# Kernel tuning notes

Hardware: AMD Instinct MI355X
Metric: run time of the kernel (lower is better)

Reference implementation:

```python
import jax, jax.numpy as jnp
import numpy as np

B, T, HS, H, R = 4, 2048, 1024, 16, 16
D = HS // H  # 64 head_dim
LOGIT_01 = float(np.log(0.1 / 0.9))    # g_proj bias init
LOGIT_098 = float(np.log(0.98 / 0.02)) # base decay logits init


def _rope_cos_sin(seq_len, dim, base=10000.0):
    half = dim // 2
    inv_freq = 1.0 / (base ** (jnp.arange(half, dtype=jnp.float32) / half))
    freqs = jnp.arange(seq_len, dtype=jnp.float32)[:, None] * inv_freq[None, :]  # [T, half]
    return jnp.cos(freqs), jnp.sin(freqs)


def _apply_rope(x, cos, sin):
    # x: [B,T,H,D] with D even; rotate interleaved pairs over full D
    c = cos[None, :, None, :]
    s = sin[None, :, None, :]
    x1 = x[..., 0::2]
    x2 = x[..., 1::2]
    r1 = x1 * c - x2 * s
    r2 = x1 * s + x2 * c
    return jnp.stack((r1, r2), axis=-1).reshape(x.shape)


def setup_inputs() -> dict:
    key = jax.random.key(0)
    ks = jax.random.split(key, 10)
    def rn(k, shape, s=0.02):
        return jax.random.normal(k, shape, dtype=jnp.float32) * s
    return {
        "x": jax.random.normal(ks[0], (B, T, HS), dtype=jnp.float32),
        "q_w": rn(ks[1], (HS, HS)),
        "k_w": rn(ks[2], (HS, HS)),
        "v_w": rn(ks[3], (HS, HS)),
        "Wq": rn(ks[4], (H, R, D), 0.05),
        "Wk": rn(ks[5], (H, R, D), 0.05),
        "g_w": rn(ks[6], (H * R, HS)),
        "g_b": jnp.full((H * R,), LOGIT_01, dtype=jnp.float32),
        "base_decay_logits": jnp.full((H, R), LOGIT_098, dtype=jnp.float32),
        "out_w": rn(ks[7], (HS, HS)),
        "out_b": jnp.zeros((HS,), dtype=jnp.float32),
        "ln_g": jnp.ones((HS,), dtype=jnp.float32),
        "ln_b": jnp.zeros((HS,), dtype=jnp.float32),
    }


def reference(x, q_w, k_w, v_w, Wq, Wk, g_w, g_b, base_decay_logits,
              out_w, out_b, ln_g, ln_b):
    b, t, hs = x.shape
    h, r, d = Wq.shape
    # qkv projections (torch Linear: x @ W.T)
    q = (x @ q_w.T).reshape(b, t, h, d)
    k = (x @ k_w.T).reshape(b, t, h, d)
    v = (x @ v_w.T).reshape(b, t, h, d)
    # RoPE (dim_rot == head_dim since it is even)
    cos, sin = _rope_cos_sin(t, d)
    q = _apply_rope(q, cos, sin)
    k = _apply_rope(k, cos, sin)
    # low-rank projections
    q_r = jnp.einsum('bthd,hrd->bthr', q, Wq)
    k_r = jnp.einsum('bthd,hrd->bthr', k, Wk)
    # content gates
    g = jax.nn.sigmoid((x @ g_w.T + g_b).reshape(b, t, h, r))
    decay = jax.nn.sigmoid(base_decay_logits)[None, :, :, None]  # [1,H,r,1]
    scale = 1.0 / jnp.sqrt(jnp.asarray(d, dtype=x.dtype))

    def step(M, inp):
        q_t, k_t, v_t, g_t = inp  # [B,H,r], [B,H,r], [B,H,D], [B,H,r]
        M = M * decay + jnp.einsum('bhr,bhd->bhrd', g_t * k_t * scale, v_t)
        y = jnp.einsum('bhr,bhrd->bhd', q_t, M)
        return M, y

    xs = (q_r.transpose(1, 0, 2, 3), k_r.transpose(1, 0, 2, 3),
          v.transpose(1, 0, 2, 3), g.transpose(1, 0, 2, 3))
    M0 = jnp.zeros((b, h, r, d), dtype=x.dtype)
    _, Y = jax.lax.scan(step, M0, xs)  # Y: [T,B,H,D]
    Y = Y.transpose(1, 0, 2, 3).reshape(b, t, hs)
    out = Y @ out_w.T + out_b  # dropout is identity at eval time
    hres = x + out
    mu = jnp.mean(hres, axis=-1, keepdims=True)
    var = jnp.mean((hres - mu) ** 2, axis=-1, keepdims=True)
    return (hres - mu) / jnp.sqrt(var + 1e-5) * ln_g + ln_b
```

## Files before the change

kernel.cpp:

```cpp
#include <hip/hip_runtime.h>
#include <hip/hip_bf16.h>

#define B_ 4
#define T_ 2048
#define HS_ 1024
#define H_ 16
#define R_ 16
#define D_ 64
#define BT_ (B_*T_)
#define NC_ 3328
#define CHUNK_ 64
#define NCHUNK_ (T_/CHUNK_)

typedef __attribute__((ext_vector_type(8))) short short8;
typedef __attribute__((ext_vector_type(4))) float f32x4;

__device__ __forceinline__ float b2f(ushort u){
    union{unsigned int i; float f;} v; v.i = ((unsigned int)u) << 16; return v.f;
}
__device__ __forceinline__ ushort f2b(float f){
    __hip_bfloat16 h = __float2bfloat16(f);
    return *reinterpret_cast<ushort*>(&h);
}
__device__ __forceinline__ float sigm(float x){ return 1.f/(1.f+expf(-x)); }

__device__ __forceinline__ void gl_lds16(const void* g, void* l){
    __builtin_amdgcn_global_load_lds((const __attribute__((address_space(1))) void*)g,
                                     (__attribute__((address_space(3))) void*)l,
                                     16, 0, 0);
}

__global__ void k_cast4(const float* __restrict__ src, ushort* __restrict__ dst){
    int i = blockIdx.x*256 + threadIdx.x;
    float4 v = ((const float4*)src)[i];
    ushort4 o; o.x=f2b(v.x); o.y=f2b(v.y); o.z=f2b(v.z); o.w=f2b(v.w);
    ((ushort4*)dst)[i] = o;
}

__global__ void k_build_wcat(const float* __restrict__ qw, const float* __restrict__ kw,
                             const float* __restrict__ vw, const float* __restrict__ gw,
                             ushort* __restrict__ wcat){
    int i = blockIdx.x*256 + threadIdx.x;
    int e = i*4;
    int row = e >> 10, col = e & 1023;
    const float* src;
    if      (row < 1024) src = qw + (size_t)row*1024 + col;
    else if (row < 2048) src = kw + (size_t)(row-1024)*1024 + col;
    else if (row < 3072) src = vw + (size_t)(row-2048)*1024 + col;
    else                 src = gw + (size_t)(row-3072)*1024 + col;
    float4 v = *(const float4*)src;
    ushort4 o; o.x=f2b(v.x); o.y=f2b(v.y); o.z=f2b(v.z); o.w=f2b(v.w);
    ((ushort4*)wcat)[i] = o;
}

__global__ void k_rope_tab(float* __restrict__ cosT, float* __restrict__ sinT){
    int i = blockIdx.x*256 + threadIdx.x;
    int t = i >> 5, f = i & 31;
    float inv = powf(10000.f, -(float)f/32.f);
    float a = (float)t * inv;
    cosT[i] = cosf(a);
    sinT[i] = sinf(a);
}

__global__ __launch_bounds__(512, 2) void k_gemm256(const ushort* __restrict__ A,
                                                    const ushort* __restrict__ Bm,
                                                    ushort* __restrict__ C,
                                                    int K, int ldc){
    __shared__ __align__(16) ushort lds[65536];
    const int tid  = threadIdx.x;
    const int lane = tid & 63, w = tid >> 6;
    const int fr = lane & 15, fg = lane >> 4;
    const int wm = w >> 2, wn = w & 3;
    const int qa = (fg + (fr >> 1)) & 3;

    int mt = gridDim.x;
    int L = blockIdx.y * mt + blockIdx.x;
    int bxi, byi;
    int msub = mt >> 3;
    if((mt & 7) == 0 && msub > 0){
        int xcd = L & 7, c = L >> 3;
        bxi = xcd * msub + (c % msub);
        byi = c / msub;
    } else { bxi = blockIdx.x; byi = blockIdx.y; }
    const long arow0 = (long)bxi * 256;
    const long brow0 = (long)byi * 256;

    const int srow = tid >> 2;
    const int scol = ((((tid & 3) - (tid >> 3)) & 3)) * 8;
    const ushort* gsrc[4];
    gsrc[0] = A  + (arow0 +       srow) * (size_t)K + scol;
    gsrc[1] = A  + (arow0 + 128 + srow) * (size_t)K + scol;
    gsrc[2] = Bm + (brow0 +       srow) * (size_t)K + scol;
    gsrc[3] = Bm + (brow0 + 128 + srow) * (size_t)K + scol;

#define STG(s, l) gl_lds16(gsrc[l] + (size_t)(s)*32, \
                           &lds[((s)&3)*16384 + (l)*4096 + w*512])

    f32x4 acc[8][4];
#pragma unroll
    for(int m=0;m<8;m++)
#pragma unroll
        for(int n=0;n<4;n++)
            acc[m][n] = (f32x4){0.f,0.f,0.f,0.f};

    const int NT = K >> 6;
#pragma unroll
    for(int s=0; s<3; ++s)
#pragma unroll
        for(int l=0; l<4; ++l) STG(s, l);

    short8 bv[4];
    for(int t=0; t<NT; ++t){
#pragma unroll
        for(int ph=0; ph<4; ++ph){
            const int ks = ph >> 1, mh = ph & 1;
            if(mh == 0) asm volatile("s_waitcnt vmcnt(8)" ::: "memory");
            __builtin_amdgcn_s_barrier();
            __builtin_amdgcn_sched_barrier(0);
            {
                const int s = 2*t + 3 + ks;
                const int l0 = mh*2;
                STG(s, l0);
                STG(s, l0+1);
            }
            const int sb = ((2*t + ks) & 3) * 16384;
            if(mh == 0){
#pragma unroll
                for(int nf=0; nf<4; ++nf){
                    int rb = (wn&1)*64 + nf*16 + fr;
                    bv[nf] = *(const short8*)&lds[sb + 8192 + rb*32 + qa*8];
                }
            }
            short8 af[4];
#pragma unroll
            for(int mm=0; mm<4; ++mm){
                int ra = wm*128 + (mh*4+mm)*16 + fr;
                af[mm] = *(const short8*)&lds[sb + ra*32 + qa*8];
            }
            __builtin_amdgcn_s_setprio(1);
#pragma unroll
            for(int mm=0; mm<4; ++mm)
#pragma unroll
            for(int nf=0; nf<4; ++nf)
                acc[mh*4+mm][nf] = __builtin_amdgcn_mfma_f32_16x16x32_bf16(
                    af[mm], bv[nf], acc[mh*4+mm][nf], 0,0,0);
            __builtin_amdgcn_s_setprio(0);
        }
    }
#undef STG
    asm volatile("s_waitcnt vmcnt(0)" ::: "memory");

#pragma unroll
    for(int m=0;m<8;m++)
#pragma unroll
        for(int n=0;n<4;n++){
            long col = brow0 + wn*64 + n*16 + fr;
#pragma unroll
            for(int j=0;j<4;j++){
                long row = arow0 + wm*128 + m*16 + fg*4 + j;
                C[row*(size_t)ldc + col] = f2b(acc[m][n][j]);
            }
        }
}

__global__ __launch_bounds__(256) void k_gemm_bt(const ushort* __restrict__ A,
                                                 const ushort* __restrict__ Bm,
                                                 ushort* __restrict__ C,
                                                 int K, int ldc){
    __shared__ __align__(16) ushort Asl[128*32];
    __shared__ __align__(16) ushort Bsl[128*32];
    int tid  = threadIdx.x;
    int lane = tid & 63, wid = tid >> 6;
    int wrow = (wid >> 1)*64, wcol = (wid & 1)*64;
    long arow0 = (long)blockIdx.x * 128;
    long brow0 = (long)blockIdx.y * 128;

    int srow = tid >> 2, sseg = (tid & 3)*8;
    const ushort* ga0 = A  + (arow0      + srow)*(size_t)K + sseg;
    const ushort* ga1 = ga0 + 64*(size_t)K;
    const ushort* gb0 = Bm + (brow0      + srow)*(size_t)K + sseg;
    const ushort* gb1 = gb0 + 64*(size_t)K;
    ushort* la0 = &Asl[(tid>>6)*512];
    ushort* la1 = la0 + 2048;
    ushort* lb0 = &Bsl[(tid>>6)*512];
    ushort* lb1 = lb0 + 2048;

    f32x4 acc[4][4];
#pragma unroll
    for(int m=0;m<4;m++)
#pragma unroll
        for(int n=0;n<4;n++)
            acc[m][n] = (f32x4){0.f,0.f,0.f,0.f};

    int fr = lane & 15, fg = lane >> 4;
    for(int kt=0; kt<K; kt+=32){
        __syncthreads();
        gl_lds16(ga0 + kt, la0);
        gl_lds16(ga1 + kt, la1);
        gl_lds16(gb0 + kt, lb0);
        gl_lds16(gb1 + kt, lb1);
        __syncthreads();

        short8 af[4], bfr[4];
#pragma unroll
        for(int m=0;m<4;m++) af[m]  = *(const short8*)&Asl[(wrow + m*16 + fr)*32 + fg*8];
#pragma unroll
        for(int n=0;n<4;n++) bfr[n] = *(const short8*)&Bsl[(wcol + n*16 + fr)*32 + fg*8];
#pragma unroll
        for(int m=0;m<4;m++)
#pragma unroll
            for(int n=0;n<4;n++)
                acc[m][n] = __builtin_amdgcn_mfma_f32_16x16x32_bf16(af[m], bfr[n], acc[m][n], 0,0,0);
    }

#pragma unroll
    for(int m=0;m<4;m++)
#pragma unroll
        for(int n=0;n<4;n++){
            long col = brow0 + wcol + n*16 + fr;
#pragma unroll
            for(int j=0;j<4;j++){
                long row = arow0 + wrow + m*16 + fg*4 + j;
                C[row*(long)ldc + col] = f2b(acc[m][n][j]);
            }
        }
}

__global__ __launch_bounds__(256) void k_rope_proj(const ushort* __restrict__ qkvg,
                                                   const float* __restrict__ cosT,
                                                   const float* __restrict__ sinT,
                                                   const float* __restrict__ Wq,
                                                   const float* __restrict__ Wk,
                                                   const float* __restrict__ gb,
                                                   float* __restrict__ qr_s,
                                                   float* __restrict__ gk_s){
    __shared__ __align__(16) ushort lq[64*72], lk[64*72];
    __shared__ __align__(16) ushort wql[16*72], wkl[16*72];
    int tid = threadIdx.x, wid = tid >> 6, lane = tid & 63;
    int bt0 = blockIdx.x * 64;
    int h   = blockIdx.y;

    {
        int row = tid >> 4, seg = tid & 15;
        float4 wq4 = *(const float4*)(Wq + (size_t)h*1024 + row*64 + seg*4);
        float4 wk4 = *(const float4*)(Wk + (size_t)h*1024 + row*64 + seg*4);
        ushort* dq = &wql[row*72 + seg*4];
        ushort* dk = &wkl[row*72 + seg*4];
        dq[0]=f2b(wq4.x); dq[1]=f2b(wq4.y); dq[2]=f2b(wq4.z); dq[3]=f2b(wq4.w);
        dk[0]=f2b(wk4.x); dk[1]=f2b(wk4.y); dk[2]=f2b(wk4.z); dk[3]=f2b(wk4.w);
    }

#pragma unroll
    for(int rep=0; rep<2; ++rep){
        int flat = rep*256 + tid;
        int row = flat >> 3, seg = flat & 7;
        int t = (bt0 + row) & 2047;
        const ushort* base = qkvg + (size_t)(bt0+row)*NC_ + h*64 + seg*8;
        short8 q8 = *(const short8*)base;
        short8 k8 = *(const short8*)(base + 1024);
        float4 cv = *(const float4*)&cosT[t*32 + seg*4];
        float4 sv = *(const float4*)&sinT[t*32 + seg*4];
        float qf[8], kf[8];
#pragma unroll
        for(int j=0;j<8;j++){ qf[j]=b2f((ushort)q8[j]); kf[j]=b2f((ushort)k8[j]); }
        float c4[4] = {cv.x,cv.y,cv.z,cv.w};
        float s4[4] = {sv.x,sv.y,sv.z,sv.w};
        short8 qo, ko;
#pragma unroll
        for(int p=0;p<4;p++){
            float c=c4[p], s=s4[p];
            qo[2*p]   = (short)f2b(qf[2*p]*c - qf[2*p+1]*s);
            qo[2*p+1] = (short)f2b(qf[2*p]*s + qf[2*p+1]*c);
            ko[2*p]   = (short)f2b(kf[2*p]*c - kf[2*p+1]*s);
            ko[2*p+1] = (short)f2b(kf[2*p]*s + kf[2*p+1]*c);
        }
        *(short8*)&lq[row*72 + seg*8] = qo;
        *(short8*)&lk[row*72 + seg*8] = ko;
    }
    __syncthreads();

    int fr = lane & 15, fg = lane >> 4;
    int wrow = wid*16;
    short8 aq0 = *(const short8*)&lq[(wrow+fr)*72 + fg*8];
    short8 aq1 = *(const short8*)&lq[(wrow+fr)*72 + 32 + fg*8];
    short8 ak0 = *(const short8*)&lk[(wrow+fr)*72 + fg*8];
    short8 ak1 = *(const short8*)&lk[(wrow+fr)*72 + 32 + fg*8];
    short8 bq0 = *(const short8*)&wql[fr*72 + fg*8];
    short8 bq1 = *(const short8*)&wql[fr*72 + 32 + fg*8];
    short8 bk0 = *(const short8*)&wkl[fr*72 + fg*8];
    short8 bk1 = *(const short8*)&wkl[fr*72 + 32 + fg*8];
    f32x4 accq = (f32x4){0.f,0.f,0.f,0.f};
    f32x4 acck = (f32x4){0.f,0.f,0.f,0.f};
    accq = __builtin_amdgcn_mfma_f32_16x16x32_bf16(aq0, bq0, accq, 0,0,0);
    accq = __builtin_amdgcn_mfma_f32_16x16x32_bf16(aq1, bq1, accq, 0,0,0);
    acck = __builtin_amdgcn_mfma_f32_16x16x32_bf16(ak0, bk0, acck, 0,0,0);
    acck = __builtin_amdgcn_mfma_f32_16x16x32_bf16(ak1, bk1, acck, 0,0,0);

    int r = fr;
    float gbv = gb[h*16 + r];
#pragma unroll
    for(int j=0;j<4;j++){
        int bt = bt0 + wrow + fg*4 + j;
        int t  = bt & 2047, b = bt >> 11;
        size_t o = (((size_t)(b*16 + h))*2048 + t)*16 + r;
        qr_s[o] = accq[j];
        float gl = b2f(qkvg[(size_t)bt*NC_ + 3072 + h*16 + r]) + gbv;
        gk_s[o] = sigm(gl) * acck[j] * 0.125f;
    }
}

__global__ __launch_bounds__(64) void k_scan_local(const ushort* __restrict__ qkvg,
                                                   const float* __restrict__ gk_s,
                                                   const float* __restrict__ bdl,
                                                   float* __restrict__ Mloc){
    int lane = threadIdx.x;
    int bx = blockIdx.x;
    int ch = bx & (NCHUNK_-1), bh = bx >> 5;
    int b = bh >> 4, h = bh & 15;
    float dec[16], M[16];
#pragma unroll
    for(int r=0;r<16;r++){ dec[r] = sigm(bdl[h*16+r]); M[r] = 0.f; }

    int t0 = ch*CHUNK_;
    const float4*  gk4 = (const float4*)(gk_s + (((size_t)bh)*2048 + t0)*16);
    const ushort*  vp  = qkvg + ((size_t)(b*2048 + t0))*NC_ + 2048 + h*64 + lane;
    for(int tt=0; tt<CHUNK_; ++tt){
        float v = b2f(*vp); vp += NC_;
        float4 a0 = gk4[0], a1 = gk4[1], a2 = gk4[2], a3 = gk4[3]; gk4 += 4;
        float gk[16] = {a0.x,a0.y,a0.z,a0.w, a1.x,a1.y,a1.z,a1.w,
                        a2.x,a2.y,a2.z,a2.w, a3.x,a3.y,a3.z,a3.w};
#pragma unroll
        for(int r=0;r<16;r++) M[r] = fmaf(M[r], dec[r], gk[r]*v);
    }
    float* mp = Mloc + ((size_t)bx)*1024 + lane;
#pragma unroll
    for(int r=0;r<16;r++) mp[r*64] = M[r];
}

__global__ __launch_bounds__(64) void k_scan_carry(float* __restrict__ Mloc,
                                                   const float* __restrict__ bdl){
    int lane = threadIdx.x;
    int sub = blockIdx.x & 3, bh = blockIdx.x >> 2, h = bh & 15;
    float decC[4], S[4];
#pragma unroll
    for(int rr=0;rr<4;rr++){
        decC[rr] = powf(sigm(bdl[h*16 + sub*4 + rr]), (float)CHUNK_);
        S[rr] = 0.f;
    }
    for(int c=0;c<NCHUNK_;c++){
        float* p = Mloc + ((size_t)(bh*NCHUNK_ + c))*1024 + lane + sub*4*64;
#pragma unroll
        for(int rr=0;rr<4;rr++){
            float m = p[rr*64];
            p[rr*64] = S[rr];
            S[rr] = fmaf(S[rr], decC[rr], m);
        }
    }
}

__global__ __launch_bounds__(64) void k_scan_out(const ushort* __restrict__ qkvg,
                                                 const float* __restrict__ gk_s,
                                                 const float* __restrict__ qr_s,
                                                 const float* __restrict__ Mst,
                                                 const float* __restrict__ bdl,
                                                 ushort* __restrict__ Ybf){
    int lane = threadIdx.x;
    int bx = blockIdx.x;
    int ch = bx & (NCHUNK_-1), bh = bx >> 5;
    int b = bh >> 4, h = bh & 15;
    float dec[16], M[16];
#pragma unroll
    for(int r=0;r<16;r++) dec[r] = sigm(bdl[h*16+r]);
    const float* sp = Mst + ((size_t)bx)*1024 + lane;
#pragma unroll
    for(int r=0;r<16;r++) M[r] = sp[r*64];

    int t0 = ch*CHUNK_;
    const float4* gk4 = (const float4*)(gk_s + (((size_t)bh)*2048 + t0)*16);
    const float4* q4  = (const float4*)(qr_s + (((size_t)bh)*2048 + t0)*16);
    const ushort* vp  = qkvg + ((size_t)(b*2048 + t0))*NC_ + 2048 + h*64 + lane;
    ushort*       yp  = Ybf  + ((size_t)(b*2048 + t0))*1024 + h*64 + lane;
    for(int tt=0; tt<CHUNK_; ++tt){
        float v = b2f(*vp); vp += NC_;
        float4 a0 = gk4[0], a1 = gk4[1], a2 = gk4[2], a3 = gk4[3]; gk4 += 4;
        float4 b0 = q4[0],  b1 = q4[1],  b2 = q4[2],  b3 = q4[3];  q4  += 4;
        float gk[16] = {a0.x,a0.y,a0.z,a0.w, a1.x,a1.y,a1.z,a1.w,
                        a2.x,a2.y,a2.z,a2.w, a3.x,a3.y,a3.z,a3.w};
        float qv[16] = {b0.x,b0.y,b0.z,b0.w, b1.x,b1.y,b1.z,b1.w,
                        b2.x,b2.y,b2.z,b2.w, b3.x,b3.y,b3.z,b3.w};
        float y = 0.f;
#pragma unroll
        for(int r=0;r<16;r++){
            M[r] = fmaf(M[r], dec[r], gk[r]*v);
            y    = fmaf(qv[r], M[r], y);
        }
        *yp = f2b(y); yp += 1024;
    }
}

__global__ __launch_bounds__(256) void k_ln(const float* __restrict__ x,
                                            const ushort* __restrict__ O,
                                            const float* __restrict__ ob,
                                            const float* __restrict__ lg,
                                            const float* __restrict__ lb,
                                            float* __restrict__ out){
    __shared__ float red[8];
    int row = blockIdx.x, tid = threadIdx.x;
    float hv[4];
    float sum = 0.f, ssq = 0.f;
#pragma unroll
    for(int k2=0;k2<4;k2++){
        int j = tid + k2*256;
        float v = x[(size_t)row*1024 + j] + b2f(O[(size_t)row*1024 + j]) + ob[j];
        hv[k2] = v; sum += v; ssq += v*v;
    }
#pragma unroll
    for(int off=32; off; off >>= 1){
        sum += __shfl_down(sum, off, 64);
        ssq += __shfl_down(ssq, off, 64);
    }
    int wid = tid >> 6, lane = tid & 63;
    if(lane == 0){ red[wid] = sum; red[4+wid] = ssq; }
    __syncthreads();
    if(tid == 0){
        float s = red[0]+red[1]+red[2]+red[3];
        float q = red[4]+red[5]+red[6]+red[7];
        float mu = s / 1024.f;
        red[0] = mu;
        red[1] = q / 1024.f - mu*mu;
    }
    __syncthreads();
    float mu = red[0];
    float inv = rsqrtf(red[1] + 1e-5f);
#pragma unroll
    for(int k2=0;k2<4;k2++){
        int j = tid + k2*256;
        out[(size_t)row*1024 + j] = (hv[k2]-mu)*inv*lg[j] + lb[j];
    }
}

extern "C" void kernel_launch(void* const* d_in, const int* in_sizes, int n_in,
                              void* d_out, int out_size, void* d_ws, size_t ws_size,
                              hipStream_t stream){
    const float* x    = (const float*)d_in[0];
    const float* q_w  = (const float*)d_in[1];
    const float* k_w  = (const float*)d_in[2];
    const float* v_w  = (const float*)d_in[3];
    const float* Wq   = (const float*)d_in[4];
    const float* Wk   = (const float*)d_in[5];
    const float* g_w  = (const float*)d_in[6];
    const float* g_b  = (const float*)d_in[7];
    const float* bdl  = (const float*)d_in[8];
    const float* outw = (const float*)d_in[9];
    const float* outb = (const float*)d_in[10];
    const float* ln_g = (const float*)d_in[11];
    const float* ln_b = (const float*)d_in[12];
    float* out = (float*)d_out;

    char* ws = (char*)d_ws;
    size_t off = 0;
    ushort* xbf  = (ushort*)(ws + off); off += (size_t)BT_*HS_*2;
    ushort* wcat = (ushort*)(ws + off); off += (size_t)NC_*HS_*2;
    ushort* owbf = (ushort*)(ws + off); off += (size_t)HS_*HS_*2;
    float*  cosT = (float*)(ws + off);  off += (size_t)T_*32*4;
    float*  sinT = (float*)(ws + off);  off += (size_t)T_*32*4;
    ushort* qkvg = (ushort*)(ws + off); off += (size_t)BT_*NC_*2;
    float*  qr_s = (float*)(ws + off);  off += (size_t)BT_*H_*R_*4;
    float*  gk_s = (float*)(ws + off);  off += (size_t)BT_*H_*R_*4;
    float*  Mloc = (float*)(ws + off);  off += (size_t)B_*H_*NCHUNK_*R_*D_*4;
    ushort* Ybf = xbf;
    ushort* O   = qkvg;

    k_cast4<<<(BT_*HS_/4)/256, 256, 0, stream>>>(x, xbf);
    k_build_wcat<<<(NC_*HS_/4)/256, 256, 0, stream>>>(q_w, k_w, v_w, g_w, wcat);
    k_cast4<<<(HS_*HS_/4)/256, 256, 0, stream>>>(outw, owbf);
    k_rope_tab<<<(T_*32)/256, 256, 0, stream>>>(cosT, sinT);

    k_gemm256<<<dim3(BT_/256, NC_/256), 512, 0, stream>>>(xbf, wcat, qkvg, HS_, NC_);

    k_rope_proj<<<dim3(BT_/64, H_), 256, 0, stream>>>(qkvg, cosT, sinT, Wq, Wk, g_b, qr_s, gk_s);

    k_scan_local<<<B_*H_*NCHUNK_, 64, 0, stream>>>(qkvg, gk_s, bdl, Mloc);
    k_scan_carry<<<B_*H_*4, 64, 0, stream>>>(Mloc, bdl);
    k_scan_out<<<B_*H_*NCHUNK_, 64, 0, stream>>>(qkvg, gk_s, qr_s, Mloc, bdl, Ybf);

    k_gemm_bt<<<dim3(BT_/128, HS_/128), 256, 0, stream>>>(Ybf, owbf, O, HS_, HS_);

    k_ln<<<BT_, 256, 0, stream>>>(x, O, outb, ln_g, ln_b, out);

    (void)in_sizes; (void)n_in; (void)out_size; (void)ws_size;
}
```

Before: 201.2 us.

## Software-pipeline LDS fragment reads one phase ahead of MFMAs in GEMM

Restructures the GEMM main loop so the A and B fragment reads from LDS for the next phase are issued before the current phase's MFMA block, using double-buffered register fragments (af0/af1, bvA/bvB). The goal is to hide LDS read latency behind matrix-core work instead of stalling on it each phase. Global-to-LDS wait counts and barrier placement are adjusted to match. In exchange, register pressure rises, and there is a risk of hazards on LDS slot reuse. The B-row index changes from (wn&1) to wn, which may alter correctness depending on the warp layout.

```diff
diff --git a/kernel.cpp b/kernel.cpp
--- a/kernel.cpp
+++ b/kernel.cpp
@@ -95,6 +95,25 @@
 
 #define STG(s, l) gl_lds16(gsrc[l] + (size_t)(s)*32, \
                            &lds[((s)&3)*16384 + (l)*4096 + w*512])
+#define RD_AF0(dst, slot) do{ const int _sb=((slot)&3)*16384;              \
+    _Pragma("unroll") for(int mm=0;mm<4;++mm){                             \
+        int ra = wm*128 + mm*16 + fr;                                      \
+        dst[mm] = *(const short8*)&lds[_sb + ra*32 + qa*8]; } }while(0)
+#define RD_AF1(dst, slot) do{ const int _sb=((slot)&3)*16384;              \
+    _Pragma("unroll") for(int mm=0;mm<4;++mm){                             \
+        int ra = wm*128 + 64 + mm*16 + fr;                                 \
+        dst[mm] = *(const short8*)&lds[_sb + ra*32 + qa*8]; } }while(0)
+#define RD_BV(dst, slot) do{ const int _sb=((slot)&3)*16384 + 8192;        \
+    _Pragma("unroll") for(int nf=0;nf<4;++nf){                             \
+        int rb = wn*64 + nf*16 + fr;                                       \
+        dst[nf] = *(const short8*)&lds[_sb + rb*32 + qa*8]; } }while(0)
+#define MFMA8(mh, afx, bvx) do{                                            \
+    __builtin_amdgcn_s_setprio(1);                                         \
+    _Pragma("unroll") for(int mm=0;mm<4;++mm)                              \
+    _Pragma("unroll") for(int nf=0;nf<4;++nf)                              \
+        acc[(mh)*4+mm][nf] = __builtin_amdgcn_mfma_f32_16x16x32_bf16(      \
+            afx[mm], bvx[nf], acc[(mh)*4+mm][nf], 0,0,0);                  \
+    __builtin_amdgcn_s_setprio(0); }while(0)
 
     f32x4 acc[8][4];
 #pragma unroll
@@ -108,47 +127,46 @@
     for(int s=0; s<3; ++s)
 #pragma unroll
         for(int l=0; l<4; ++l) STG(s, l);
-
-    short8 bv[4];
+    asm volatile("s_waitcnt vmcnt(8)" ::: "memory");
+    __builtin_amdgcn_s_barrier();
+    __builtin_amdgcn_sched_barrier(0);
+
+    short8 af0[4], af1[4], bvA[4], bvB[4];
+    RD_BV(bvA, 0);
+    RD_AF0(af0, 0);
+
     for(int t=0; t<NT; ++t){
-#pragma unroll
-        for(int ph=0; ph<4; ++ph){
-            const int ks = ph >> 1, mh = ph & 1;
-            if(mh == 0) asm volatile("s_waitcnt vmcnt(8)" ::: "memory");
-            __builtin_amdgcn_s_barrier();
-            __builtin_amdgcn_sched_barrier(0);
-            {
-                const int s = 2*t + 3 + ks;
-                const int l0 = mh*2;
-                STG(s, l0);
-                STG(s, l0+1);
-            }
-            const int sb = ((2*t + ks) & 3) * 16384;
-            if(mh == 0){
-#pragma unroll
-                for(int nf=0; nf<4; ++nf){
-                    int rb = (wn&1)*64 + nf*16 + fr;
-                    bv[nf] = *(const short8*)&lds[sb + 8192 + rb*32 + qa*8];
-                }
-            }
-            short8 af[4];
-#pragma unroll
-            for(int mm=0; mm<4; ++mm){
-                int ra = wm*128 + (mh*4+mm)*16 + fr;
-                af[mm] = *(const short8*)&lds[sb + ra*32 + qa*8];
-            }
-            __builtin_amdgcn_s_setprio(1);
-#pragma unroll
-            for(int mm=0; mm<4; ++mm)
-#pragma unroll
-            for(int nf=0; nf<4; ++nf)
-                acc[mh*4+mm][nf] = __builtin_amdgcn_mfma_f32_16x16x32_bf16(
-                    af[mm], bv[nf], acc[mh*4+mm][nf], 0,0,0);
-            __builtin_amdgcn_s_setprio(0);
-        }
-    }
+        __builtin_amdgcn_s_barrier();
+        __builtin_amdgcn_sched_barrier(0);
+        STG(2*t+3, 0); STG(2*t+3, 1);
+        RD_AF1(af1, 2*t);
+        MFMA8(0, af0, bvA);
+        asm volatile("s_waitcnt vmcnt(6)" ::: "memory");
+        __builtin_amdgcn_s_barrier();
+        __builtin_amdgcn_sched_barrier(0);
+        STG(2*t+3, 2); STG(2*t+3, 3);
+        RD_BV(bvB, 2*t+1);
+        RD_AF0(af0, 2*t+1);
+        MFMA8(1, af1, bvA);
+        __builtin_amdgcn_s_barrier();
+        __builtin_amdgcn_sched_barrier(0);
+        STG(2*t+4, 0); STG(2*t+4, 1);
+        RD_AF1(af1, 2*t+1);
+        MFMA8(0, af0, bvB);
+        asm volatile("s_waitcnt vmcnt(6)" ::: "memory");
+        __builtin_amdgcn_s_barrier();
+        __builtin_amdgcn_sched_barrier(0);
+        STG(2*t+4, 2); STG(2*t+4, 3);
+        RD_BV(bvA, 2*t+2);
+        RD_AF0(af0, 2*t+2);
+        MFMA8(1, af1, bvB);
+    }
+    asm volatile("s_waitcnt vmcnt(0)" ::: "memory");
 #undef STG
-    asm volatile("s_waitcnt vmcnt(0)" ::: "memory");
+#undef RD_AF0
+#undef RD_AF1
+#undef RD_BV
+#undef MFMA8
 
 #pragma unroll
     for(int m=0;m<8;m++)
```

Result: no change. 200.1 us (-0.6%).
